# Kernel optimization log

Hardware: AMD Instinct MI355X
Metric: run time of the kernel (lower is better)

Reference implementation:

```python
import jax, jax.numpy as jnp
import numpy as np

# Model config (mirrors init_kwargs)
E = 8          # num_experts
K = 2          # top_k
S = 1          # select_top_k
THRESHOLD = 0.7
NORM_TOPK = True
H = 1024       # hidden_dim
F = 1024       # moe intermediate dim
B, SEQ = 2, 1024


def setup_inputs() -> dict:
    key = jax.random.key(0)
    k1, k2, k3, k4, k5 = jax.random.split(key, 5)
    hidden_states = jax.random.normal(k1, (B, SEQ, H), jnp.float32)
    gate_weight = jax.random.normal(k2, (E, H), jnp.float32) * 0.02
    gate_up_proj = jax.random.normal(k3, (E, 2 * F, H), jnp.float32) * 0.02
    down_proj = jax.random.normal(k4, (E, H, F), jnp.float32) * 0.02
    sim = jax.random.uniform(k5, (E, E), jnp.float32)
    sim = (sim + sim.T) / 2.0
    sim = sim.at[jnp.arange(E), jnp.arange(E)].set(1.0)  # fill_diagonal_(1.0)
    return {
        "hidden_states": hidden_states,
        "gate_weight": gate_weight,
        "gate_up_proj": gate_up_proj,
        "down_proj": down_proj,
        "similarity_matrix": sim,
    }


def reference(hidden_states, gate_weight, gate_up_proj, down_proj, similarity_matrix):
    b, s, h = hidden_states.shape
    x = hidden_states.reshape(-1, h)                     # [N, H]
    N = x.shape[0]

    # Router: logits -> softmax(fp32) -> topk (+ optional norm)
    logits = x @ gate_weight.T                           # [N, E]
    probs = jax.nn.softmax(logits.astype(jnp.float32), axis=-1)
    top_w, top_i = jax.lax.top_k(probs, K)               # [N, K]
    if NORM_TOPK:
        top_w = top_w / jnp.clip(jnp.sum(top_w, -1, keepdims=True), 1e-12)

    # SERE reroute: primary = union of top-S experts over batch; map each
    # secondary expert to its most-similar primary if sim >= threshold.
    primary_mask = jnp.zeros((E,), bool).at[top_i[:, :S].reshape(-1)].set(True)
    sim = jnp.where(primary_mask[None, :], similarity_matrix.astype(jnp.float32), -jnp.inf)
    best_j = jnp.argmax(sim, axis=-1)                    # best primary per expert
    best_sim = jnp.max(sim, axis=-1)
    ids = jnp.arange(E)
    expert_map = jnp.where((~primary_mask) & (best_sim >= THRESHOLD), best_j, ids)
    rerouted = expert_map[top_i]                         # [N, K]

    # Merge duplicate slots via scatter-add, then re-topk K.
    rows = jnp.arange(N)[:, None]
    dense = jnp.zeros((N, E), top_w.dtype).at[rows, rerouted].add(top_w)
    fw, fi = jax.lax.top_k(dense, K)                     # nnz per row <= K, so topk keeps all
    combine = jnp.zeros((N, E), fw.dtype).at[rows, fi].add(jnp.where(fw > 0, fw, 0.0))  # [N, E]

    # Expert MLPs (dense jit-friendly dispatch): silu(gate)*up -> down
    gu = jnp.einsum('nh,efh->enf', x, gate_up_proj)      # [E, N, 2F]
    g, u = jnp.split(gu, 2, axis=-1)
    hmid = jax.nn.silu(g) * u                            # [E, N, F]
    y = jnp.einsum('enf,ehf->enh', hmid, down_proj)      # [E, N, H]
    out = jnp.einsum('ne,enh->nh', combine, y)           # weighted combine
    return out.reshape(b, s, h)
```

## Files before the change

### kernel.cpp

```cpp
#include <hip/hip_runtime.h>
#include <cstdint>
#include <cstddef>

#define N_TOK 2048
#define HID 1024
#define FDIM 1024
#define NE 8
#define PAIR_CAP 5120
#define MT 128
#define BK 64
#define THRESH 0.7f

typedef __attribute__((ext_vector_type(8))) short bf16x8;
typedef __attribute__((ext_vector_type(4))) float f32x4;

static __device__ __forceinline__ unsigned short f2bf(float f) {
  unsigned int u = __float_as_uint(f);
  u += 0x7FFF + ((u >> 16) & 1);
  return (unsigned short)(u >> 16);
}
static __device__ __forceinline__ float bf2f(unsigned short u) {
  return __uint_as_float(((unsigned int)u) << 16);
}

static __device__ __forceinline__ void gl2lds16(const unsigned short* g, unsigned short* l) {
  __builtin_amdgcn_global_load_lds(
      (const __attribute__((address_space(1))) void*)g,
      (__attribute__((address_space(3))) void*)l, 16, 0, 0);
}

__global__ __launch_bounds__(256) void k_cvt(
    const float* __restrict__ src, unsigned short* __restrict__ dst, int n4) {
  int i = blockIdx.x * 256 + threadIdx.x;
  if (i < n4) {
    float4 v = ((const float4*)src)[i];
    ushort4 o;
    o.x = f2bf(v.x); o.y = f2bf(v.y); o.z = f2bf(v.z); o.w = f2bf(v.w);
    ((ushort4*)dst)[i] = o;
  }
}

__global__ __launch_bounds__(256) void k_router(
    const float* __restrict__ x, const float* __restrict__ gw,
    unsigned short* __restrict__ xb, float* __restrict__ topw,
    int* __restrict__ topi) {
  __shared__ float sgw[NE * HID];
  int t = threadIdx.x;
#pragma unroll
  for (int i = 0; i < NE * HID / 256; ++i) sgw[t + 256 * i] = gw[t + 256 * i];
  __syncthreads();
  int lane = t & 63;
  int wave = t >> 6;
  int n = blockIdx.x * 4 + wave;
  float acc[NE];
#pragma unroll
  for (int e = 0; e < NE; ++e) acc[e] = 0.f;
#pragma unroll
  for (int i = 0; i < HID / 64; ++i) {
    int h = i * 64 + lane;
    float xv = x[(size_t)n * HID + h];
    xb[(size_t)n * HID + h] = f2bf(xv);
#pragma unroll
    for (int e = 0; e < NE; ++e) acc[e] += xv * sgw[e * HID + h];
  }
#pragma unroll
  for (int off = 32; off > 0; off >>= 1) {
#pragma unroll
    for (int e = 0; e < NE; ++e) acc[e] += __shfl_xor(acc[e], off, 64);
  }
  if (lane == 0) {
    float m = acc[0];
    for (int e = 1; e < NE; ++e) m = fmaxf(m, acc[e]);
    float p[NE]; float s = 0.f;
    for (int e = 0; e < NE; ++e) { p[e] = __expf(acc[e] - m); s += p[e]; }
    float inv = 1.f / s;
    for (int e = 0; e < NE; ++e) p[e] *= inv;
    int i0 = 0; float b0 = p[0];
    for (int e = 1; e < NE; ++e) if (p[e] > b0) { b0 = p[e]; i0 = e; }
    int i1 = -1; float b1 = -1.f;
    for (int e = 0; e < NE; ++e) { if (e == i0) continue; if (p[e] > b1) { b1 = p[e]; i1 = e; } }
    float sw = b0 + b1; if (sw < 1e-12f) sw = 1e-12f;
    topw[n * 2] = b0 / sw; topw[n * 2 + 1] = b1 / sw;
    topi[n * 2] = i0;      topi[n * 2 + 1] = i1;
  }
}

__global__ __launch_bounds__(256) void k_pairs(
    const float* __restrict__ sim, const int* __restrict__ topi,
    const float* __restrict__ topw, int* __restrict__ ctrl,
    int* __restrict__ ptok, float* __restrict__ pw, int* __restrict__ pot) {
  __shared__ int prim[NE], emap[NE], cnt[NE], soff[NE], cur[NE], padc[NE];
  int t = threadIdx.x;
  if (t < NE) { prim[t] = 0; cnt[t] = 0; }
  __syncthreads();
  for (int n = t; n < N_TOK; n += 256) prim[topi[n * 2]] = 1;
  __syncthreads();
  if (t < NE) {
    float best = -1e30f; int bj = -1;
    for (int j = 0; j < NE; ++j) {
      if (prim[j]) {
        float s = sim[t * NE + j];
        if (s > best) { best = s; bj = j; }
      }
    }
    int m = t;
    if (!prim[t] && bj >= 0 && best >= THRESH) m = bj;
    emap[t] = m;
  }
  __syncthreads();
  for (int n = t; n < N_TOK; n += 256) {
    atomicAdd(&cnt[emap[topi[n * 2]]], 1);
    atomicAdd(&cnt[emap[topi[n * 2 + 1]]], 1);
  }
  __syncthreads();
  if (t == 0) {
    int o = 0;
    for (int e = 0; e < NE; ++e) {
      soff[e] = o;
      int p = (cnt[e] + MT - 1) & ~(MT - 1);
      padc[e] = p; cur[e] = 0; o += p;
    }
  }
  __syncthreads();
  if (t < NE) { ctrl[24 + t] = soff[t]; ctrl[32 + t] = padc[t]; }
  for (int n = t; n < N_TOK; n += 256) {
    int i0 = topi[n * 2], i1 = topi[n * 2 + 1];
    int e0 = emap[i0], e1 = emap[i1];
    int s0 = soff[e0] + atomicAdd(&cur[e0], 1);
    int s1 = soff[e1] + atomicAdd(&cur[e1], 1);
    ptok[s0] = n; pw[s0] = topw[n * 2];
    ptok[s1] = n; pw[s1] = topw[n * 2 + 1];
    pot[n * 2] = s0; pot[n * 2 + 1] = s1;
  }
  __syncthreads();
  for (int e = 0; e < NE; ++e) {
    for (int s = cnt[e] + t; s < padc[e]; s += 256) {
      ptok[soff[e] + s] = 0; pw[soff[e] + s] = 0.f;
    }
  }
}


__global__ __launch_bounds__(256, 2) void k_gemm1(
    const unsigned short* __restrict__ xb, const unsigned short* __restrict__ gupb,
    unsigned short* __restrict__ hmid, const int* __restrict__ ptok,
    const int* __restrict__ ctrl) {
  int b = blockIdx.x;
  int mt = b >> 8;
  int r8 = b & 255;
  int e = r8 >> 5;
  int y = r8 & 31;
  int padc = ctrl[32 + e];
  if (mt * MT >= padc) return;
  int base = ctrl[24 + e] + mt * MT;
  int f0 = y * 32;

  __shared__ unsigned short As[MT * BK];
  __shared__ unsigned short Bs[64 * BK];
  __shared__ int toks[MT];

  int t = threadIdx.x;
  if (t < MT) toks[t] = ptok[base + t];
  __syncthreads();

  int lane = t & 63;
  int wave = t >> 6;
  int wm = wave >> 1, wn = wave & 1;
  int lm = lane & 15, lh = lane >> 4;

  f32x4 acc[4][2] = {};
  const unsigned short* gbase = gupb + (size_t)e * 2 * FDIM * HID;

  for (int k0 = 0; k0 < HID; k0 += BK) {
#pragma unroll
    for (int i = 0; i < 4; ++i) {
      int q = i * 256 + t;
      int r = q >> 3;
      int cl = (q & 7) ^ (r & 7);
      gl2lds16(xb + (size_t)toks[r] * HID + k0 + cl * 8, &As[(q & ~63) * 8]);
    }
#pragma unroll
    for (int i = 0; i < 2; ++i) {
      int q = i * 256 + t;
      int r = q >> 3;
      int cl = (q & 7) ^ (r & 7);
      int grow = ((r >> 4) & 1) * FDIM + f0 + ((r >> 5) << 4) + (r & 15);
      gl2lds16(gbase + (size_t)grow * HID + k0 + cl * 8, &Bs[(q & ~63) * 8]);
    }
    __syncthreads();
#pragma unroll
    for (int kk = 0; kk < 2; ++kk) {
      bf16x8 af[4], bfr[2];
#pragma unroll
      for (int rb = 0; rb < 4; ++rb) {
        int row = wm * 64 + rb * 16 + lm;
        int p = (kk * 4 + lh) ^ (row & 7);
        af[rb] = *(const bf16x8*)(&As[row * BK + p * 8]);
      }
#pragma unroll
      for (int cc = 0; cc < 2; ++cc) {
        int row = wn * 32 + cc * 16 + lm;
        int p = (kk * 4 + lh) ^ (row & 7);
        bfr[cc] = *(const bf16x8*)(&Bs[row * BK + p * 8]);
      }
#pragma unroll
      for (int rb = 0; rb < 4; ++rb) {
#pragma unroll
        for (int cc = 0; cc < 2; ++cc)
          acc[rb][cc] = __builtin_amdgcn_mfma_f32_16x16x32_bf16(af[rb], bfr[cc], acc[rb][cc], 0, 0, 0);
      }
    }
    __syncthreads();
  }
#pragma unroll
  for (int rb = 0; rb < 4; ++rb) {
    int slot = base + wm * 64 + rb * 16 + lh * 4;
    f32x4 g = acc[rb][0];
    f32x4 u = acc[rb][1];
    int f = f0 + wn * 16 + lm;
#pragma unroll
    for (int reg = 0; reg < 4; ++reg) {
      float gv = g[reg];
      float hm = gv / (1.f + __expf(-gv)) * u[reg];
      hmid[(size_t)(slot + reg) * FDIM + f] = f2bf(hm);
    }
  }
}

__global__ __launch_bounds__(256, 2) void k_gemm2(
    const unsigned short* __restrict__ hmid, const unsigned short* __restrict__ dwnb,
    unsigned short* __restrict__ yb, const int* __restrict__ ctrl) {
  int b = blockIdx.x;
  int mt = b >> 8;
  int r8 = b & 255;
  int e = r8 >> 5;
  int y = r8 & 31;
  int padc = ctrl[32 + e];
  if (mt * MT >= padc) return;
  int base = ctrl[24 + e] + mt * MT;
  int h0 = y * 32;

  __shared__ unsigned short As[MT * BK];
  __shared__ unsigned short Bs[32 * BK];

  int t = threadIdx.x;
  int lane = t & 63;
  int wave = t >> 6;
  int wm = wave >> 1, wn = wave & 1;
  int lm = lane & 15, lh = lane >> 4;

  f32x4 acc[4] = {};
  const unsigned short* dbase = dwnb + (size_t)e * HID * FDIM;

  for (int k0 = 0; k0 < FDIM; k0 += BK) {
#pragma unroll
    for (int i = 0; i < 4; ++i) {
      int q = i * 256 + t;
      int r = q >> 3;
      int cl = (q & 7) ^ (r & 7);
      gl2lds16(hmid + (size_t)(base + r) * FDIM + k0 + cl * 8, &As[(q & ~63) * 8]);
    }
    {
      int q = t;
      int r = q >> 3;
      int cl = (q & 7) ^ (r & 7);
      gl2lds16(dbase + (size_t)(h0 + r) * FDIM + k0 + cl * 8, &Bs[(q & ~63) * 8]);
    }
    __syncthreads();
#pragma unroll
    for (int kk = 0; kk < 2; ++kk) {
      bf16x8 af[4], bfr;
#pragma unroll
      for (int rb = 0; rb < 4; ++rb) {
        int row = wm * 64 + rb * 16 + lm;
        int p = (kk * 4 + lh) ^ (row & 7);
        af[rb] = *(const bf16x8*)(&As[row * BK + p * 8]);
      }
      {
        int row = wn * 16 + lm;
        int p = (kk * 4 + lh) ^ (row & 7);
        bfr = *(const bf16x8*)(&Bs[row * BK + p * 8]);
      }
#pragma unroll
      for (int rb = 0; rb < 4; ++rb)
        acc[rb] = __builtin_amdgcn_mfma_f32_16x16x32_bf16(af[rb], bfr, acc[rb], 0, 0, 0);
    }
    __syncthreads();
  }
#pragma unroll
  for (int rb = 0; rb < 4; ++rb) {
    int slot = base + wm * 64 + rb * 16 + lh * 4;
    int h = h0 + wn * 16 + lm;
#pragma unroll
    for (int reg = 0; reg < 4; ++reg)
      yb[(size_t)(slot + reg) * HID + h] = f2bf(acc[rb][reg]);
  }
}

__global__ __launch_bounds__(256) void k_combine(
    const unsigned short* __restrict__ yb, const float* __restrict__ pw,
    const int* __restrict__ pot, float* __restrict__ out) {
  int n = blockIdx.x;
  int t = threadIdx.x;
  int p0 = pot[n * 2], p1 = pot[n * 2 + 1];
  float w0 = pw[p0], w1 = pw[p1];
  int h = t * 4;
  ushort4 a = *(const ushort4*)(yb + (size_t)p0 * HID + h);
  ushort4 b = *(const ushort4*)(yb + (size_t)p1 * HID + h);
  float4 o;
  o.x = w0 * bf2f(a.x) + w1 * bf2f(b.x);
  o.y = w0 * bf2f(a.y) + w1 * bf2f(b.y);
  o.z = w0 * bf2f(a.z) + w1 * bf2f(b.z);
  o.w = w0 * bf2f(a.w) + w1 * bf2f(b.w);
  *(float4*)(out + (size_t)n * HID + h) = o;
}

extern "C" void kernel_launch(void* const* d_in, const int* in_sizes, int n_in,
                              void* d_out, int out_size, void* d_ws, size_t ws_size,
                              hipStream_t stream) {
  (void)in_sizes; (void)n_in; (void)out_size; (void)ws_size;
  const float* x   = (const float*)d_in[0];
  const float* gw  = (const float*)d_in[1];
  const float* gup = (const float*)d_in[2];
  const float* dwn = (const float*)d_in[3];
  const float* sim = (const float*)d_in[4];
  float* out = (float*)d_out;

  char* w = (char*)d_ws;
  int* ctrl = (int*)w;
  size_t off = 256;
  unsigned short* xb = (unsigned short*)(w + off); off += (size_t)N_TOK * HID * 2;
  float* topw = (float*)(w + off); off += (size_t)N_TOK * 2 * 4;
  int*   topi = (int*)(w + off);   off += (size_t)N_TOK * 2 * 4;
  int*   ptok = (int*)(w + off);   off += (size_t)PAIR_CAP * 4;
  float* pw   = (float*)(w + off); off += (size_t)PAIR_CAP * 4;
  int*   pot  = (int*)(w + off);   off += (size_t)N_TOK * 2 * 4;
  unsigned short* hmid = (unsigned short*)(w + off); off += (size_t)PAIR_CAP * FDIM * 2;
  unsigned short* yb   = (unsigned short*)(w + off); off += (size_t)PAIR_CAP * HID * 2;
  unsigned short* gupb = (unsigned short*)(w + off); off += (size_t)NE * 2 * FDIM * HID * 2;
  unsigned short* dwnb = (unsigned short*)(w + off); off += (size_t)NE * HID * FDIM * 2;

  int n4g = NE * 2 * FDIM * HID / 4;
  int n4d = NE * HID * FDIM / 4;
  k_cvt<<<(n4g + 255) / 256, 256, 0, stream>>>(gup, gupb, n4g);
  k_cvt<<<(n4d + 255) / 256, 256, 0, stream>>>(dwn, dwnb, n4d);
  k_router<<<N_TOK / 4, 256, 0, stream>>>(x, gw, xb, topw, topi);
  k_pairs<<<1, 256, 0, stream>>>(sim, topi, topw, ctrl, ptok, pw, pot);
  k_gemm1<<<dim3(32 * 256), 256, 0, stream>>>(xb, gupb, hmid, ptok, ctrl);
  k_gemm2<<<dim3(32 * 256), 256, 0, stream>>>(hmid, dwnb, yb, ctrl);
  k_combine<<<N_TOK, 256, 0, stream>>>(yb, pw, pot, out);
}
```

Measured before the change: 212.6 us.

## Double-buffer LDS tiles in expert GEMMs and compact grid to active tiles

Both expert GEMM kernels now double-buffer their LDS A/B tiles, prefetching two k-steps ahead with manual vmcnt waits, so global loads overlap MFMA work. The routing kernel also writes the total tile count and a per-tile expert table. The GEMM grids shrink from 8192 blocks, most exiting early, to 1280 blocks indexed directly by tile. In exchange LDS use per block doubles, and the hand-written waitcnt counts must match the exact number of loads issued per stage.

```diff
diff --git a/kernel.cpp b/kernel.cpp
--- a/kernel.cpp
+++ b/kernel.cpp
@@ -120,9 +120,17 @@
       int p = (cnt[e] + MT - 1) & ~(MT - 1);
       padc[e] = p; cur[e] = 0; o += p;
     }
+    ctrl[1] = o >> 7;
   }
   __syncthreads();
   if (t < NE) { ctrl[24 + t] = soff[t]; ctrl[32 + t] = padc[t]; }
+  if (t < 40) {
+    int slot = t << 7;
+    int e = 0;
+    for (int j = 0; j < NE; ++j)
+      if (slot >= soff[j] && slot < soff[j] + padc[j]) e = j;
+    ctrl[64 + t] = e;
+  }
   for (int n = t; n < N_TOK; n += 256) {
     int i0 = topi[n * 2], i1 = topi[n * 2 + 1];
     int e0 = emap[i0], e1 = emap[i1];
@@ -146,17 +154,15 @@
     unsigned short* __restrict__ hmid, const int* __restrict__ ptok,
     const int* __restrict__ ctrl) {
   int b = blockIdx.x;
-  int mt = b >> 8;
-  int r8 = b & 255;
-  int e = r8 >> 5;
-  int y = r8 & 31;
-  int padc = ctrl[32 + e];
-  if (mt * MT >= padc) return;
-  int base = ctrl[24 + e] + mt * MT;
+  int tl = b >> 5;
+  int y = b & 31;
+  if (tl >= ctrl[1]) return;
+  int e = ctrl[64 + tl];
+  int base = tl * MT;
   int f0 = y * 32;
 
-  __shared__ unsigned short As[MT * BK];
-  __shared__ unsigned short Bs[64 * BK];
+  __shared__ unsigned short As[2][MT * BK];
+  __shared__ unsigned short Bs[2][64 * BK];
   __shared__ int toks[MT];
 
   int t = threadIdx.x;
@@ -171,13 +177,13 @@
   f32x4 acc[4][2] = {};
   const unsigned short* gbase = gupb + (size_t)e * 2 * FDIM * HID;
 
-  for (int k0 = 0; k0 < HID; k0 += BK) {
+  auto stage = [&](int k0, int bi) {
 #pragma unroll
     for (int i = 0; i < 4; ++i) {
       int q = i * 256 + t;
       int r = q >> 3;
       int cl = (q & 7) ^ (r & 7);
-      gl2lds16(xb + (size_t)toks[r] * HID + k0 + cl * 8, &As[(q & ~63) * 8]);
+      gl2lds16(xb + (size_t)toks[r] * HID + k0 + cl * 8, &As[bi][(q & ~63) * 8]);
     }
 #pragma unroll
     for (int i = 0; i < 2; ++i) {
@@ -185,9 +191,18 @@
       int r = q >> 3;
       int cl = (q & 7) ^ (r & 7);
       int grow = ((r >> 4) & 1) * FDIM + f0 + ((r >> 5) << 4) + (r & 15);
-      gl2lds16(gbase + (size_t)grow * HID + k0 + cl * 8, &Bs[(q & ~63) * 8]);
-    }
-    __syncthreads();
+      gl2lds16(gbase + (size_t)grow * HID + k0 + cl * 8, &Bs[bi][(q & ~63) * 8]);
+    }
+  };
+
+  stage(0, 0);
+  stage(BK, 1);
+
+  for (int k = 0; k < 16; ++k) {
+    if (k < 15) asm volatile("s_waitcnt vmcnt(6)" ::: "memory");
+    else        asm volatile("s_waitcnt vmcnt(0)" ::: "memory");
+    asm volatile("s_barrier" ::: "memory");
+    int bi = k & 1;
 #pragma unroll
     for (int kk = 0; kk < 2; ++kk) {
       bf16x8 af[4], bfr[2];
@@ -195,13 +210,13 @@
       for (int rb = 0; rb < 4; ++rb) {
         int row = wm * 64 + rb * 16 + lm;
         int p = (kk * 4 + lh) ^ (row & 7);
-        af[rb] = *(const bf16x8*)(&As[row * BK + p * 8]);
+        af[rb] = *(const bf16x8*)(&As[bi][row * BK + p * 8]);
       }
 #pragma unroll
       for (int cc = 0; cc < 2; ++cc) {
         int row = wn * 32 + cc * 16 + lm;
         int p = (kk * 4 + lh) ^ (row & 7);
-        bfr[cc] = *(const bf16x8*)(&Bs[row * BK + p * 8]);
+        bfr[cc] = *(const bf16x8*)(&Bs[bi][row * BK + p * 8]);
       }
 #pragma unroll
       for (int rb = 0; rb < 4; ++rb) {
@@ -210,7 +225,11 @@
           acc[rb][cc] = __builtin_amdgcn_mfma_f32_16x16x32_bf16(af[rb], bfr[cc], acc[rb][cc], 0, 0, 0);
       }
     }
-    __syncthreads();
+    if (k < 14) {
+      asm volatile("s_waitcnt lgkmcnt(0)" ::: "memory");
+      asm volatile("s_barrier" ::: "memory");
+      stage((k + 2) * BK, bi);
+    }
   }
 #pragma unroll
   for (int rb = 0; rb < 4; ++rb) {
@@ -231,17 +250,15 @@
     const unsigned short* __restrict__ hmid, const unsigned short* __restrict__ dwnb,
     unsigned short* __restrict__ yb, const int* __restrict__ ctrl) {
   int b = blockIdx.x;
-  int mt = b >> 8;
-  int r8 = b & 255;
-  int e = r8 >> 5;
-  int y = r8 & 31;
-  int padc = ctrl[32 + e];
-  if (mt * MT >= padc) return;
-  int base = ctrl[24 + e] + mt * MT;
+  int tl = b >> 5;
+  int y = b & 31;
+  if (tl >= ctrl[1]) return;
+  int e = ctrl[64 + tl];
+  int base = tl * MT;
   int h0 = y * 32;
 
-  __shared__ unsigned short As[MT * BK];
-  __shared__ unsigned short Bs[32 * BK];
+  __shared__ unsigned short As[2][MT * BK];
+  __shared__ unsigned short Bs[2][32 * BK];
 
   int t = threadIdx.x;
   int lane = t & 63;
@@ -252,21 +269,30 @@
   f32x4 acc[4] = {};
   const unsigned short* dbase = dwnb + (size_t)e * HID * FDIM;
 
-  for (int k0 = 0; k0 < FDIM; k0 += BK) {
+  auto stage = [&](int k0, int bi) {
 #pragma unroll
     for (int i = 0; i < 4; ++i) {
       int q = i * 256 + t;
       int r = q >> 3;
       int cl = (q & 7) ^ (r & 7);
-      gl2lds16(hmid + (size_t)(base + r) * FDIM + k0 + cl * 8, &As[(q & ~63) * 8]);
+      gl2lds16(hmid + (size_t)(base + r) * FDIM + k0 + cl * 8, &As[bi][(q & ~63) * 8]);
     }
     {
       int q = t;
       int r = q >> 3;
       int cl = (q & 7) ^ (r & 7);
-      gl2lds16(dbase + (size_t)(h0 + r) * FDIM + k0 + cl * 8, &Bs[(q & ~63) * 8]);
-    }
-    __syncthreads();
+      gl2lds16(dbase + (size_t)(h0 + r) * FDIM + k0 + cl * 8, &Bs[bi][(q & ~63) * 8]);
+    }
+  };
+
+  stage(0, 0);
+  stage(BK, 1);
+
+  for (int k = 0; k < 16; ++k) {
+    if (k < 15) asm volatile("s_waitcnt vmcnt(5)" ::: "memory");
+    else        asm volatile("s_waitcnt vmcnt(0)" ::: "memory");
+    asm volatile("s_barrier" ::: "memory");
+    int bi = k & 1;
 #pragma unroll
     for (int kk = 0; kk < 2; ++kk) {
       bf16x8 af[4], bfr;
@@ -274,18 +300,22 @@
       for (int rb = 0; rb < 4; ++rb) {
         int row = wm * 64 + rb * 16 + lm;
         int p = (kk * 4 + lh) ^ (row & 7);
-        af[rb] = *(const bf16x8*)(&As[row * BK + p * 8]);
+        af[rb] = *(const bf16x8*)(&As[bi][row * BK + p * 8]);
       }
       {
         int row = wn * 16 + lm;
         int p = (kk * 4 + lh) ^ (row & 7);
-        bfr = *(const bf16x8*)(&Bs[row * BK + p * 8]);
+        bfr = *(const bf16x8*)(&Bs[bi][row * BK + p * 8]);
       }
 #pragma unroll
       for (int rb = 0; rb < 4; ++rb)
         acc[rb] = __builtin_amdgcn_mfma_f32_16x16x32_bf16(af[rb], bfr, acc[rb], 0, 0, 0);
     }
-    __syncthreads();
+    if (k < 14) {
+      asm volatile("s_waitcnt lgkmcnt(0)" ::: "memory");
+      asm volatile("s_barrier" ::: "memory");
+      stage((k + 2) * BK, bi);
+    }
   }
 #pragma unroll
   for (int rb = 0; rb < 4; ++rb) {
@@ -328,7 +358,7 @@
 
   char* w = (char*)d_ws;
   int* ctrl = (int*)w;
-  size_t off = 256;
+  size_t off = 512;
   unsigned short* xb = (unsigned short*)(w + off); off += (size_t)N_TOK * HID * 2;
   float* topw = (float*)(w + off); off += (size_t)N_TOK * 2 * 4;
   int*   topi = (int*)(w + off);   off += (size_t)N_TOK * 2 * 4;
@@ -346,7 +376,7 @@
   k_cvt<<<(n4d + 255) / 256, 256, 0, stream>>>(dwn, dwnb, n4d);
   k_router<<<N_TOK / 4, 256, 0, stream>>>(x, gw, xb, topw, topi);
   k_pairs<<<1, 256, 0, stream>>>(sim, topi, topw, ctrl, ptok, pw, pot);
-  k_gemm1<<<dim3(32 * 256), 256, 0, stream>>>(xb, gupb, hmid, ptok, ctrl);
-  k_gemm2<<<dim3(32 * 256), 256, 0, stream>>>(hmid, dwnb, yb, ctrl);
+  k_gemm1<<<dim3(40 * 32), 256, 0, stream>>>(xb, gupb, hmid, ptok, ctrl);
+  k_gemm2<<<dim3(40 * 32), 256, 0, stream>>>(hmid, dwnb, yb, ctrl);
   k_combine<<<N_TOK, 256, 0, stream>>>(yb, pw, pot, out);
 }
```

Result: no change. 214.1 us (+0.7%).
